# Kernel tuning notes

Measured on AMD Instinct MI355X. Metric: run time of the kernel, lower is better.

## Reference

```python
import jax, jax.numpy as jnp
import numpy as np

H = 1024       # hidden_dim
NH = 16        # num_attention_heads
HD = H // NH   # head_dim = 64
ROT = 32       # rotary_dim
MP = 8         # MP_NUM hardcoded in forward
NEG_INF = jnp.float32(-1e9)


def setup_inputs() -> dict:
    key = jax.random.key(0)
    k1, k2, k3 = jax.random.split(key, 3)
    hidden_states = jax.random.normal(k1, (2, 2048, H), dtype=jnp.float32)
    w_qkv = jax.random.normal(k2, (H, 3 * H), dtype=jnp.float32) * 0.02
    w_out = jax.random.normal(k3, (H, H), dtype=jnp.float32) * 0.02
    return {"hidden_states": hidden_states, "w_qkv": w_qkv, "w_out": w_out}


def _rotate_every_two(x):
    # GPT-J rotate: (x0,x1,x2,x3,...) -> (-x1,x0,-x3,x2,...)
    x1 = x[..., ::2]
    x2 = x[..., 1::2]
    return jnp.stack((-x2, x1), axis=-1).reshape(x.shape)


def _apply_rope(x, sin, cos):
    return x * cos + _rotate_every_two(x) * sin


def reference(hidden_states, w_qkv, w_out):
    B, S, _ = hidden_states.shape
    qkv = hidden_states @ w_qkv                      # [B,S,3H]
    qkv = qkv.reshape(B, S, MP, 3 * H // MP)         # GPT-J MP-split layout
    local = NH * HD // MP
    q = qkv[..., :local]
    k = qkv[..., local:2 * local]
    v = qkv[..., 2 * local:]

    def split_heads(x):  # [B,S,MP,H/MP] -> [B,S,NH,HD]
        return x.reshape(B, S, MP, NH // MP, HD).reshape(B, S, NH, HD)

    q, k, v = split_heads(q), split_heads(k), split_heads(v)

    # fixed position embedding (GPT-J), offset=0, seq dim = 1
    inv_freq = 1.0 / (10000.0 ** (jnp.arange(0, ROT, 2, dtype=jnp.float32) / ROT))
    sinusoid = jnp.einsum('i,j->ij', jnp.arange(S, dtype=jnp.float32), inv_freq)  # [S,ROT/2]
    sin = jnp.repeat(jnp.sin(sinusoid), 2, axis=-1)[None, :, None, :]             # [1,S,1,ROT]
    cos = jnp.repeat(jnp.cos(sinusoid), 2, axis=-1)[None, :, None, :]

    q = jnp.concatenate([_apply_rope(q[..., :ROT], sin, cos), q[..., ROT:]], axis=-1)
    k = jnp.concatenate([_apply_rope(k[..., :ROT], sin, cos), k[..., ROT:]], axis=-1)

    q = q.transpose(0, 2, 1, 3)  # [B,NH,S,HD]
    k = k.transpose(0, 2, 1, 3)
    v = v.transpose(0, 2, 1, 3)

    # manual causal attention in fp32 (as the torch code casts q,k to fp32)
    scores = jnp.einsum('bhqd,bhkd->bhqk', q, k) / jnp.sqrt(jnp.float32(HD))
    causal = jnp.tril(jnp.ones((S, S), dtype=bool))[None, None]
    scores = jnp.where(causal, scores, NEG_INF)
    probs = jax.nn.softmax(scores, axis=-1)
    attn = jnp.einsum('bhqk,bhkd->bhqd', probs, v)   # [B,NH,S,HD]

    attn = attn.transpose(0, 2, 1, 3).reshape(B, S, H)  # merge heads
    return attn @ w_out
```

## Files before the change

kernel.cpp:

```cpp
#include <hip/hip_runtime.h>

#define SEQ   2048
#define NHEADS 16
#define HDIM  64
#define HID   1024
#define ROT   32

typedef __attribute__((ext_vector_type(8))) short  short8;
typedef __attribute__((ext_vector_type(4))) float  floatx4;

__device__ __forceinline__ ushort f2bf(float f) {
    union { float f; uint u; } v; v.f = f;
    uint x = v.u;
    uint r = (x + 0x7FFFu + ((x >> 16) & 1u)) >> 16;
    return (ushort)r;
}

__device__ __forceinline__ float fexp2(float x) {
    return __builtin_amdgcn_exp2f(x);
}

__device__ __forceinline__ floatx4 mfma_bf16(short8 a, short8 b, floatx4 c) {
    return __builtin_amdgcn_mfma_f32_16x16x32_bf16(a, b, c, 0, 0, 0);
}

__device__ __forceinline__ void gload16(const ushort* g, ushort* l) {
    __builtin_amdgcn_global_load_lds(
        (const __attribute__((address_space(1))) void*)g,
        (__attribute__((address_space(3))) void*)l, 16, 0, 0);
}

__global__ __launch_bounds__(256) void convert_bf16_kernel(
    const float* __restrict__ src, ushort* __restrict__ dst, int n)
{
    int i = (blockIdx.x * 256 + threadIdx.x) * 8;
    if (i >= n) return;
    float4 a = *(const float4*)(src + i);
    float4 b = *(const float4*)(src + i + 4);
    short8 v;
    v[0] = (short)f2bf(a.x); v[1] = (short)f2bf(a.y);
    v[2] = (short)f2bf(a.z); v[3] = (short)f2bf(a.w);
    v[4] = (short)f2bf(b.x); v[5] = (short)f2bf(b.y);
    v[6] = (short)f2bf(b.z); v[7] = (short)f2bf(b.w);
    *(short8*)(dst + i) = v;
}

__global__ __launch_bounds__(256) void transpose_bf16_kernel(
    const float* __restrict__ src, ushort* __restrict__ dst, int K, int N)
{
    __shared__ ushort Tl[64 * 68];
    const int k0 = blockIdx.y * 64, n0 = blockIdx.x * 64;
    const int tid = threadIdx.x;
    #pragma unroll
    for (int i = 0; i < 4; i++) {
        int lin = tid + 256 * i;
        int row = lin >> 4;
        int c4  = (lin & 15) * 4;
        float4 v = *(const float4*)(src + (size_t)(k0 + row) * N + n0 + c4);
        uint2 u;
        u.x = (uint)f2bf(v.x) | ((uint)f2bf(v.y) << 16);
        u.y = (uint)f2bf(v.z) | ((uint)f2bf(v.w) << 16);
        *(uint2*)&Tl[row * 68 + c4] = u;
    }
    __syncthreads();
    #pragma unroll
    for (int j = 0; j < 2; j++) {
        int lin = tid + 256 * j;
        int n = lin >> 3, c = lin & 7;
        short8 v;
        #pragma unroll
        for (int u = 0; u < 8; u++) v[u] = (short)Tl[(c * 8 + u) * 68 + n];
        *(short8*)(dst + (size_t)(n0 + n) * K + k0 + c * 8) = v;
    }
}

__global__ __launch_bounds__(512) void qkv_rope_kernel(
    const ushort* __restrict__ hbf,
    const ushort* __restrict__ wqkvT,
    ushort* __restrict__ Qb, ushort* __restrict__ Kb, ushort* __restrict__ Vb)
{
    __shared__ ushort Al[2][4096];
    __shared__ ushort Bl[2][8192];
    const int tid  = threadIdx.x;
    const int lane = tid & 63;
    const int wv   = tid >> 6;
    const int g    = lane >> 4;
    const int l15  = lane & 15;

    const int lin  = blockIdx.x + 12 * blockIdx.y;
    const int xcd  = lin & 7;
    const int slot = lin >> 3;
    const int cxi  = xcd & 1, cyi = xcd >> 1;
    const int sx   = slot % 6, sy = slot / 6;
    const int n0   = (cxi * 6 + sx) * 256;
    const int m0   = (cyi * 8 + sy) * 128;

    const int wr = (wv >> 2) * 64;
    const int wc = (wv & 3) * 64;
    const int arow = tid >> 2;
    const int acol = (tid & 3) * 8;

    floatx4 acc[4][4];
    #pragma unroll
    for (int a = 0; a < 4; a++)
        #pragma unroll
        for (int bq = 0; bq < 4; bq++)
            acc[a][bq] = floatx4{0.f, 0.f, 0.f, 0.f};

    const ushort* ga  = hbf   + (size_t)(m0 + arow) * 1024 + acol;
    const ushort* gb0 = wqkvT + (size_t)(n0 + arow) * 1024 + acol;
    const ushort* gb1 = gb0 + (size_t)128 * 1024;
    const int wofs = wv * 512;

    auto stage = [&](int t, int buf) {
        const int k0 = t * 32;
        gload16(ga  + k0, &Al[buf][wofs]);
        gload16(gb0 + k0, &Bl[buf][wofs]);
        gload16(gb1 + k0, &Bl[buf][4096 + wofs]);
    };

    stage(0, 0);
    asm volatile("s_waitcnt vmcnt(0)" ::: "memory");
    __builtin_amdgcn_s_barrier();

    for (int it = 0; it < 32; it++) {
        const int cur = it & 1;
        if (it + 1 < 32) stage(it + 1, cur ^ 1);
        short8 af[4], bfr[4];
        #pragma unroll
        for (int fm = 0; fm < 4; fm++)
            af[fm] = *(const short8*)&Al[cur][(wr + fm * 16 + l15) * 32 + g * 8];
        #pragma unroll
        for (int fn = 0; fn < 4; fn++)
            bfr[fn] = *(const short8*)&Bl[cur][(wc + fn * 16 + l15) * 32 + g * 8];
        #pragma unroll
        for (int fm = 0; fm < 4; fm++)
            #pragma unroll
            for (int fn = 0; fn < 4; fn++)
                acc[fm][fn] = mfma_bf16(af[fm], bfr[fn], acc[fm][fn]);
        asm volatile("s_waitcnt vmcnt(0)" ::: "memory");
        __builtin_amdgcn_s_barrier();
    }

    #pragma unroll
    for (int fn = 0; fn < 4; fn++) {
        const int c    = n0 + wc + fn * 16 + l15;
        const int mp   = c / 384;
        const int rem  = c - mp * 384;
        const int tsel = rem >> 7;
        const int j    = (rem >> 6) & 1;
        const int d    = rem & 63;
        const int head = mp * 2 + j;
        ushort* basep = (tsel == 0) ? Qb : (tsel == 1) ? Kb : Vb;
        const bool rope = (tsel < 2) && (d < ROT);
        const float qscale = (tsel == 0) ? 0.18033688011112042f : 1.0f;
        float freq = 0.f;
        if (rope) {
            freq = exp2f((float)(d >> 1) * -0.830482023721841f);
        }
        #pragma unroll
        for (int fm = 0; fm < 4; fm++) {
            #pragma unroll
            for (int r = 0; r < 4; r++) {
                int row = m0 + wr + fm * 16 + g * 4 + r;
                int bb  = row >> 11;
                int s   = row & 2047;
                float val = acc[fm][fn][r];
                float pv  = __shfl_xor(val, 1, 64);
                float outv = val;
                if (rope) {
                    float ang = (float)s * freq;
                    float sn, cs;
                    __sincosf(ang, &sn, &cs);
                    outv = ((d & 1) == 0) ? (val * cs - pv * sn)
                                          : (val * cs + pv * sn);
                }
                outv *= qscale;
                size_t off;
                if (tsel == 2)
                    off = ((size_t)(bb * NHEADS + head) * HDIM + d) * SEQ + s;
                else
                    off = ((size_t)(bb * NHEADS + head) * SEQ + s) * HDIM + d;
                basep[off] = f2bf(outv);
            }
        }
    }
}

__global__ __launch_bounds__(512, 4) void attn_kernel(
    const ushort* __restrict__ Qb, const ushort* __restrict__ Kb,
    const ushort* __restrict__ Vb, ushort* __restrict__ attn)
{
    __shared__ ushort Kl[2][64 * 72];
    __shared__ ushort Vt[2][64 * 72];

    const int tid  = threadIdx.x;
    const int lane = tid & 63;
    const int wv   = tid >> 6;
    const int g    = lane >> 4;
    const int l15  = lane & 15;

    const int l    = blockIdx.x + 16 * blockIdx.y + 256 * blockIdx.z;
    const int half = l >> 8;
    const int xx   = l & 15;
    const int hh   = (l >> 4) & 15;
    const int qb   = half ? xx : 15 - xx;
    const int bb   = half;

    const int q0 = qb * 128;
    const int wq = wv * 16;
    const size_t kvbase = (size_t)(bb * NHEADS + hh) * SEQ * HDIM;

    const int srow = tid >> 3;
    const int sch  = (tid & 7) * 8;

    short8 qreg[2];
    #pragma unroll
    for (int ks = 0; ks < 2; ks++)
        qreg[ks] = *(const short8*)(Qb + kvbase +
            (size_t)(q0 + wq + l15) * HDIM + ks * 32 + g * 8);

    float m = -__builtin_inff();
    float lsum = 0.f;
    floatx4 of[4];
    #pragma unroll
    for (int df = 0; df < 4; df++) of[df] = floatx4{0.f, 0.f, 0.f, 0.f};

    const int nt = 2 * qb + 2;

    auto load_tile = [&](int tt, short8& kr, short8& vr) {
        const int kv = tt * 64;
        kr = *(const short8*)(Kb + kvbase + (size_t)(kv + srow) * HDIM + sch);
        vr = *(const short8*)(Vb + kvbase + (size_t)srow * SEQ + kv + sch);
    };
    auto write_tile = [&](int buf, short8& kr, short8& vr) {
        *(short8*)&Kl[buf][srow * 72 + sch] = kr;
        *(short8*)&Vt[buf][srow * 72 + sch] = vr;
    };
    auto compute_tile = [&](int t, const ushort* Kc, const ushort* Vc) {
        const int kv0 = t * 64;
        if (kv0 > q0 + wq + 15) return;
        floatx4 sf[4];
        __builtin_amdgcn_s_setprio(1);
        #pragma unroll
        for (int kf = 0; kf < 4; kf++) {
            short8 kr0 = *(const short8*)&Kc[(kf * 16 + l15) * 72 + g * 8];
            short8 kr1 = *(const short8*)&Kc[(kf * 16 + l15) * 72 + 32 + g * 8];
            floatx4 s = floatx4{0.f, 0.f, 0.f, 0.f};
            s = mfma_bf16(kr0, qreg[0], s);
            s = mfma_bf16(kr1, qreg[1], s);
            sf[kf] = s;
        }
        __builtin_amdgcn_s_setprio(0);

        const bool diag = (kv0 + 63 > q0 + wq);
        const int qg = q0 + wq + l15;
        float tmax = -__builtin_inff();
        if (diag) {
            #pragma unroll
            for (int kf = 0; kf < 4; kf++) {
                #pragma unroll
                for (int r = 0; r < 4; r++) {
                    int key = kv0 + kf * 16 + g * 4 + r;
                    float x = sf[kf][r];
                    if (key > qg) x = -1e9f;
                    sf[kf][r] = x;
                    tmax = fmaxf(tmax, x);
                }
            }
        } else {
            #pragma unroll
            for (int kf = 0; kf < 4; kf++)
                #pragma unroll
                for (int r = 0; r < 4; r++)
                    tmax = fmaxf(tmax, sf[kf][r]);
        }
        if (!__all(tmax <= m + 8.0f)) {
            tmax = fmaxf(tmax, __shfl_xor(tmax, 16, 64));
            tmax = fmaxf(tmax, __shfl_xor(tmax, 32, 64));
            float mn = fmaxf(m, tmax);
            float f  = fexp2(m - mn);
            m = mn;
            lsum *= f;
            #pragma unroll
            for (int r = 0; r < 4; r++) {
                float fr = __shfl(f, g * 4 + r, 64);
                #pragma unroll
                for (int df = 0; df < 4; df++)
                    of[df][r] *= fr;
            }
        }
        float rs = 0.f;
        #pragma unroll
        for (int kf = 0; kf < 4; kf++) {
            #pragma unroll
            for (int r = 0; r < 4; r++) {
                float p = fexp2(sf[kf][r] - m);
                sf[kf][r] = p;
                rs += p;
            }
        }
        lsum += rs;
        short8 pa[2];
        #pragma unroll
        for (int ks = 0; ks < 2; ks++) {
            union { short8 s; uint u[4]; } pu;
            #pragma unroll
            for (int w = 0; w < 4; w++) {
                const int kf = 2 * ks + (w >> 1);
                float lo = sf[kf][(w & 1) * 2 + 0];
                float hi = sf[kf][(w & 1) * 2 + 1];
                asm("v_cvt_pk_bf16_f32 %0, %1, %2"
                    : "=v"(pu.u[w]) : "v"(lo), "v"(hi));
            }
            pa[ks] = pu.s;
        }
        __builtin_amdgcn_s_setprio(1);
        #pragma unroll
        for (int df = 0; df < 4; df++) {
            #pragma unroll
            for (int ks = 0; ks < 2; ks++) {
                const int vb = (df * 16 + l15) * 72 + ks * 32 + g * 4;
                uint2 v0 = *(const uint2*)&Vc[vb];
                uint2 v1 = *(const uint2*)&Vc[vb + 16];
                union { short8 s; uint4 u; } vv;
                vv.u.x = v0.x; vv.u.y = v0.y; vv.u.z = v1.x; vv.u.w = v1.y;
                of[df] = mfma_bf16(pa[ks], vv.s, of[df]);
            }
        }
        __builtin_amdgcn_s_setprio(0);
    };

    short8 kA, vA, kB, vB;
    load_tile(0, kA, vA);
    if (nt > 1) load_tile(1, kB, vB);
    write_tile(0, kA, vA);
    __syncthreads();

    for (int t = 0; t < nt; t += 2) {
        if (t + 2 < nt) load_tile(t + 2, kA, vA);
        compute_tile(t, Kl[0], Vt[0]);
        write_tile(1, kB, vB);
        __syncthreads();
        if (t + 3 < nt) load_tile(t + 3, kB, vB);
        compute_tile(t + 1, Kl[1], Vt[1]);
        if (t + 2 < nt) write_tile(0, kA, vA);
        __syncthreads();
    }

    lsum += __shfl_xor(lsum, 16, 64);
    lsum += __shfl_xor(lsum, 32, 64);
    #pragma unroll
    for (int r = 0; r < 4; r++) {
        float lr = __shfl(lsum, g * 4 + r, 64);
        float inv = 1.0f / lr;
        int q = q0 + wq + g * 4 + r;
        #pragma unroll
        for (int df = 0; df < 4; df++)
            attn[((size_t)bb * SEQ + q) * HID + hh * 64 + df * 16 + l15] =
                f2bf(of[df][r] * inv);
    }
}

__global__ __launch_bounds__(256) void out_proj_kernel(
    const ushort* __restrict__ attn,
    const ushort* __restrict__ woutT,
    float* __restrict__ out)
{
    __shared__ ushort Al[2][128 * 32];
    __shared__ ushort Bl[2][128 * 32];
    const int tid  = threadIdx.x;
    const int lane = tid & 63;
    const int wv   = tid >> 6;
    const int g    = lane >> 4;
    const int l15  = lane & 15;

    const int lin  = blockIdx.x + 8 * blockIdx.y;
    const int xcd  = lin & 7;
    const int slot = lin >> 3;
    const int cxi  = xcd & 1, cyi = xcd >> 1;
    const int sx   = slot & 3, sy = slot >> 2;
    const int n0   = (cxi * 4 + sx) * 128;
    const int m0   = (cyi * 8 + sy) * 128;

    const int wr = (wv >> 1) * 64;
    const int wc = (wv & 1) * 64;
    const int rowl = lane >> 2;
    const int kcol = (lane & 3) * 8;

    floatx4 acc[4][4];
    #pragma unroll
    for (int a = 0; a < 4; a++)
        #pragma unroll
        for (int bq = 0; bq < 4; bq++)
            acc[a][bq] = floatx4{0.f, 0.f, 0.f, 0.f};

    const ushort* ga = attn  + (size_t)(m0 + wv * 32 + rowl) * 1024 + kcol;
    const ushort* gb = woutT + (size_t)(n0 + wv * 32 + rowl) * 1024 + kcol;
    const int lofs = wv * 1024;

    gload16(ga,             &Al[0][lofs]);
    gload16(ga + 16 * 1024, &Al[0][lofs + 512]);
    gload16(gb,             &Bl[0][lofs]);
    gload16(gb + 16 * 1024, &Bl[0][lofs + 512]);
    asm volatile("s_waitcnt vmcnt(0)" ::: "memory");
    __builtin_amdgcn_s_barrier();

    for (int it = 0; it < 32; it++) {
        const int cur = it & 1;
        if (it + 1 < 32) {
            const int k0 = (it + 1) * 32;
            const int nxt = cur ^ 1;
            gload16(ga + k0,             &Al[nxt][lofs]);
            gload16(ga + k0 + 16 * 1024, &Al[nxt][lofs + 512]);
            gload16(gb + k0,             &Bl[nxt][lofs]);
            gload16(gb + k0 + 16 * 1024, &Bl[nxt][lofs + 512]);
        }
        short8 af[4], bfr[4];
        #pragma unroll
        for (int fm = 0; fm < 4; fm++)
            af[fm] = *(const short8*)&Al[cur][(wr + fm * 16 + l15) * 32 + g * 8];
        #pragma unroll
        for (int fn = 0; fn < 4; fn++)
            bfr[fn] = *(const short8*)&Bl[cur][(wc + fn * 16 + l15) * 32 + g * 8];
        #pragma unroll
        for (int fm = 0; fm < 4; fm++)
            #pragma unroll
            for (int fn = 0; fn < 4; fn++)
                acc[fm][fn] = mfma_bf16(af[fm], bfr[fn], acc[fm][fn]);
        asm volatile("s_waitcnt vmcnt(0)" ::: "memory");
        __builtin_amdgcn_s_barrier();
    }
    #pragma unroll
    for (int fm = 0; fm < 4; fm++)
        #pragma unroll
        for (int fn = 0; fn < 4; fn++)
            #pragma unroll
            for (int r = 0; r < 4; r++) {
                int row = m0 + wr + fm * 16 + g * 4 + r;
                int col = n0 + wc + fn * 16 + l15;
                out[(size_t)row * 1024 + col] = acc[fm][fn][r];
            }
}

extern "C" void kernel_launch(void* const* d_in, const int* in_sizes, int n_in,
                              void* d_out, int out_size, void* d_ws, size_t ws_size,
                              hipStream_t stream)
{
    const float* hidden = (const float*)d_in[0];
    const float* wqkv   = (const float*)d_in[1];
    const float* wout   = (const float*)d_in[2];
    float* out = (float*)d_out;

    const size_t NELEM = (size_t)2 * SEQ * HID;
    ushort* Qb    = (ushort*)d_ws;
    ushort* Kb    = Qb + NELEM;
    ushort* Vb    = Kb + NELEM;
    ushort* hbf   = Vb + NELEM;
    ushort* wqkvT = hbf + NELEM;
    ushort* woutT = wqkvT + (size_t)3072 * 1024;
    ushort* attnb = hbf;

    convert_bf16_kernel<<<2048, 256, 0, stream>>>(hidden, hbf, (int)NELEM);
    transpose_bf16_kernel<<<dim3(48, 16), 256, 0, stream>>>(wqkv, wqkvT, 1024, 3072);
    transpose_bf16_kernel<<<dim3(16, 16), 256, 0, stream>>>(wout, woutT, 1024, 1024);
    qkv_rope_kernel<<<dim3(12, 32), 512, 0, stream>>>(hbf, wqkvT, Qb, Kb, Vb);
    attn_kernel<<<dim3(16, NHEADS, 2), 512, 0, stream>>>(Qb, Kb, Vb, attnb);
    out_proj_kernel<<<dim3(8, 32), 256, 0, stream>>>(attnb, woutT, out);
}
```

Measured before the change: 129.4 us.

## Enlarge QKV GEMM tile to 256x256 with triple-buffered LDS prefetch

The QKV projection GEMM tile grows from 128x256 to 256x256 per block, with each wave now computing a 128x64 sub-tile (8x4 MFMA fragments). This halves the grid to 192 blocks and raises data reuse per LDS load. LDS staging moves from double to triple buffering, prefetching two K-steps ahead with partial vmcnt waits so loads overlap compute more fully. The cost is doubled accumulator registers and fewer blocks than the 256 CUs, which leaves some CUs idle and lowers occupancy.

New measurement: 144.4 us. 1.12x slower.

```diff
diff --git a/kernel.cpp b/kernel.cpp
--- a/kernel.cpp
+++ b/kernel.cpp
@@ -79,8 +79,8 @@
     const ushort* __restrict__ wqkvT,
     ushort* __restrict__ Qb, ushort* __restrict__ Kb, ushort* __restrict__ Vb)
 {
-    __shared__ ushort Al[2][4096];
-    __shared__ ushort Bl[2][8192];
+    __shared__ ushort Al[3 * 8192];
+    __shared__ ushort Bl[3 * 8192];
     const int tid  = threadIdx.x;
     const int lane = tid & 63;
     const int wv   = tid >> 6;
@@ -93,53 +93,55 @@
     const int cxi  = xcd & 1, cyi = xcd >> 1;
     const int sx   = slot % 6, sy = slot / 6;
     const int n0   = (cxi * 6 + sx) * 256;
-    const int m0   = (cyi * 8 + sy) * 128;
-
-    const int wr = (wv >> 2) * 64;
+    const int m0   = (cyi * 4 + sy) * 256;
+
+    const int wr = (wv >> 2) * 128;
     const int wc = (wv & 3) * 64;
-    const int arow = tid >> 2;
-    const int acol = (tid & 3) * 8;
-
-    floatx4 acc[4][4];
-    #pragma unroll
-    for (int a = 0; a < 4; a++)
+
+    floatx4 acc[8][4];
+    #pragma unroll
+    for (int a = 0; a < 8; a++)
         #pragma unroll
         for (int bq = 0; bq < 4; bq++)
             acc[a][bq] = floatx4{0.f, 0.f, 0.f, 0.f};
 
-    const ushort* ga  = hbf   + (size_t)(m0 + arow) * 1024 + acol;
-    const ushort* gb0 = wqkvT + (size_t)(n0 + arow) * 1024 + acol;
-    const ushort* gb1 = gb0 + (size_t)128 * 1024;
-    const int wofs = wv * 512;
-
-    auto stage = [&](int t, int buf) {
+    const ushort* ga = hbf   + (size_t)(m0 + (tid >> 2)) * 1024 + (tid & 3) * 8;
+    const ushort* gb = wqkvT + (size_t)(n0 + (tid >> 2)) * 1024 + (tid & 3) * 8;
+    const int lofs = tid * 8;
+
+    auto stage = [&](int t, int obuf) {
         const int k0 = t * 32;
-        gload16(ga  + k0, &Al[buf][wofs]);
-        gload16(gb0 + k0, &Bl[buf][wofs]);
-        gload16(gb1 + k0, &Bl[buf][4096 + wofs]);
+        gload16(ga + k0,                &Al[obuf + lofs]);
+        gload16(ga + k0 + 128 * 1024,   &Al[obuf + lofs + 4096]);
+        gload16(gb + k0,                &Bl[obuf + lofs]);
+        gload16(gb + k0 + 128 * 1024,   &Bl[obuf + lofs + 4096]);
     };
 
-    stage(0, 0);
-    asm volatile("s_waitcnt vmcnt(0)" ::: "memory");
+    int o0 = 0, o1 = 8192, o2 = 16384;
+    stage(0, o0);
+    stage(1, o1);
+    asm volatile("s_waitcnt vmcnt(4)" ::: "memory");
     __builtin_amdgcn_s_barrier();
 
     for (int it = 0; it < 32; it++) {
-        const int cur = it & 1;
-        if (it + 1 < 32) stage(it + 1, cur ^ 1);
-        short8 af[4], bfr[4];
-        #pragma unroll
-        for (int fm = 0; fm < 4; fm++)
-            af[fm] = *(const short8*)&Al[cur][(wr + fm * 16 + l15) * 32 + g * 8];
+        const bool pre = (it + 2 < 32);
+        if (pre) stage(it + 2, o2);
+        short8 af[8], bfr[4];
+        #pragma unroll
+        for (int fm = 0; fm < 8; fm++)
+            af[fm] = *(const short8*)&Al[o0 + (wr + fm * 16 + l15) * 32 + g * 8];
         #pragma unroll
         for (int fn = 0; fn < 4; fn++)
-            bfr[fn] = *(const short8*)&Bl[cur][(wc + fn * 16 + l15) * 32 + g * 8];
-        #pragma unroll
-        for (int fm = 0; fm < 4; fm++)
+            bfr[fn] = *(const short8*)&Bl[o0 + (wc + fn * 16 + l15) * 32 + g * 8];
+        #pragma unroll
+        for (int fm = 0; fm < 8; fm++)
             #pragma unroll
             for (int fn = 0; fn < 4; fn++)
                 acc[fm][fn] = mfma_bf16(af[fm], bfr[fn], acc[fm][fn]);
-        asm volatile("s_waitcnt vmcnt(0)" ::: "memory");
+        if (pre) asm volatile("s_waitcnt vmcnt(4)" ::: "memory");
+        else     asm volatile("s_waitcnt vmcnt(0)" ::: "memory");
         __builtin_amdgcn_s_barrier();
+        int tmp = o0; o0 = o1; o1 = o2; o2 = tmp;
     }
 
     #pragma unroll
@@ -159,7 +161,7 @@
             freq = exp2f((float)(d >> 1) * -0.830482023721841f);
         }
         #pragma unroll
-        for (int fm = 0; fm < 4; fm++) {
+        for (int fm = 0; fm < 8; fm++) {
             #pragma unroll
             for (int r = 0; r < 4; r++) {
                 int row = m0 + wr + fm * 16 + g * 4 + r;
@@ -464,7 +466,7 @@
     convert_bf16_kernel<<<2048, 256, 0, stream>>>(hidden, hbf, (int)NELEM);
     transpose_bf16_kernel<<<dim3(48, 16), 256, 0, stream>>>(wqkv, wqkvT, 1024, 3072);
     transpose_bf16_kernel<<<dim3(16, 16), 256, 0, stream>>>(wout, woutT, 1024, 1024);
-    qkv_rope_kernel<<<dim3(12, 32), 512, 0, stream>>>(hbf, wqkvT, Qb, Kb, Vb);
+    qkv_rope_kernel<<<dim3(12, 16), 512, 0, stream>>>(hbf, wqkvT, Qb, Kb, Vb);
     attn_kernel<<<dim3(16, NHEADS, 2), 512, 0, stream>>>(Qb, Kb, Vb, attnb);
     out_proj_kernel<<<dim3(8, 32), 256, 0, stream>>>(attnb, woutT, out);
 }
```
